# Optimization experiments

Hardware: AMD Instinct MI355X
Metric: run time of the kernel (lower is better)

The kernel has to match this reference:

```python
import jax, jax.numpy as jnp
import numpy as np

B, T, D, H = 2, 2048, 1024, 16
HD = D // H
ALPHA = HD ** -0.5
EPS = 1e-5


def setup_inputs() -> dict:
    key = jax.random.key(0)
    ks = jax.random.split(key, 8)
    x = jax.random.normal(ks[0], (B, T, D), dtype=jnp.float32)
    # additive causal mask: 0 where allowed, -inf where disallowed
    causal = jnp.triu(jnp.ones((T, T), dtype=bool), k=1)
    attention_mask = jnp.where(causal, -jnp.inf, 0.0).astype(jnp.float32)
    rab = jax.random.normal(ks[1], (1, H, T, T), dtype=jnp.float32) * 0.02
    W_in = jax.random.normal(ks[2], (D, 4 * D), dtype=jnp.float32) * (D ** -0.5)
    b_in = jnp.zeros((4 * D,), dtype=jnp.float32)
    W_out = jax.random.normal(ks[3], (D, D), dtype=jnp.float32) * (D ** -0.5)
    b_out = jnp.zeros((D,), dtype=jnp.float32)
    ln_w = jnp.ones((D,), dtype=jnp.float32)
    ln_b = jnp.zeros((D,), dtype=jnp.float32)
    return {"x": x, "attention_mask": attention_mask, "rab": rab,
            "W_in": W_in, "b_in": b_in, "W_out": W_out, "b_out": b_out,
            "ln_w": ln_w, "ln_b": ln_b}


def _heads(t):  # [B,T,D] -> [B,H,T,HD]
    return t.reshape(B, T, H, HD).transpose(0, 2, 1, 3)


def _layernorm(t, w, b):
    mu = jnp.mean(t, axis=-1, keepdims=True)
    var = jnp.mean(jnp.square(t - mu), axis=-1, keepdims=True)
    return (t - mu) * jax.lax.rsqrt(var + EPS) * w + b


def reference(x, attention_mask, rab, W_in, b_in, W_out, b_out, ln_w, ln_b):
    h = jax.nn.silu(x @ W_in + b_in)                      # [B,T,4D]
    U, V, Q, K = jnp.split(h, 4, axis=-1)
    Qh, Kh, Vh = _heads(Q), _heads(K), _heads(V)
    logits = jnp.einsum('bhqd,bhkd->bhqk', Qh, Kh) * ALPHA
    logits = logits + rab + attention_mask[None, None]    # [B,H,T,T]
    # allowed counts from the additive mask (0 == allowed)
    allowed = (attention_mask == 0).astype(jnp.float32)   # [T,T]
    denom = jnp.clip(jnp.sum(allowed, axis=-1, keepdims=True), 1.0)  # [T,1]
    logits_safe = jnp.where(jnp.isinf(logits) & (logits < 0), -1e9, logits)
    attn = jax.nn.silu(logits_safe) / denom[None, None]
    AV = jnp.einsum('bhqk,bhkd->bhqd', attn, Vh)
    AV = AV.transpose(0, 2, 1, 3).reshape(B, T, D)
    y = (_layernorm(AV, ln_w, ln_b) * U) @ W_out + b_out
    return y
```

## Files before the change

### kernel.cpp

```cpp
#include <hip/hip_runtime.h>
#include <hip/hip_bf16.h>

#define BATCH 2
#define TSEQ 2048
#define DIM 1024
#define NH 16
#define HDIM 64
#define MROWS (BATCH * TSEQ)

typedef __attribute__((ext_vector_type(4))) float f32x4;
typedef __attribute__((ext_vector_type(8))) short short8;

__device__ __forceinline__ unsigned short f2bf(float f) {
    union { float f; unsigned int u; } x; x.f = f;
    unsigned int r = x.u + 0x7fffu + ((x.u >> 16) & 1u);
    return (unsigned short)(r >> 16);
}

__device__ __forceinline__ float bf2f(unsigned short s) {
    union { unsigned int u; float f; } t; t.u = (unsigned int)s << 16;
    return t.f;
}

__device__ __forceinline__ float silu_f(float v) {
    return v * __builtin_amdgcn_rcpf(1.f + __expf(-v));
}

__device__ __forceinline__ unsigned int pack_bf16(float lo, float hi) {
    union { __hip_bfloat162 h; unsigned int u; } r;
    r.h = __float22bfloat162_rn(float2{lo, hi});
    return r.u;
}

__device__ __forceinline__ void gl_lds16(const void* g, void* l) {
    __builtin_amdgcn_global_load_lds(
        (const __attribute__((address_space(1))) void*)g,
        (__attribute__((address_space(3))) void*)l, 16, 0, 0);
}

__device__ __forceinline__ short8 rd_swz(const unsigned short* base, int row, int chunk) {
    const char* b = (const char*)base;
    return *(const short8*)(b + row * 128 + (((chunk ^ (row & 7)) << 4)));
}

__global__ __launch_bounds__(256) void k_convert(const float* __restrict__ in,
                                                 unsigned short* __restrict__ out,
                                                 int n4) {
    int i = blockIdx.x * 256 + threadIdx.x;
    if (i < n4) {
        float4 v = ((const float4*)in)[i];
        union { unsigned short s[4]; uint2 u; } o;
        o.s[0] = f2bf(v.x); o.s[1] = f2bf(v.y); o.s[2] = f2bf(v.z); o.s[3] = f2bf(v.w);
        ((uint2*)out)[i] = o.u;
    }
}

__global__ __launch_bounds__(256) void k_transpose(const float* __restrict__ in,
                                                   unsigned short* __restrict__ out,
                                                   int R, int C) {
    __shared__ float tile[32][33];
    int tx = threadIdx.x, ty = threadIdx.y;
    int c0 = blockIdx.x * 32, r0 = blockIdx.y * 32;
    #pragma unroll
    for (int i = 0; i < 32; i += 8)
        tile[ty + i][tx] = in[(size_t)(r0 + ty + i) * C + c0 + tx];
    __syncthreads();
    #pragma unroll
    for (int i = 0; i < 32; i += 8)
        out[(size_t)(c0 + ty + i) * R + r0 + tx] = f2bf(tile[tx][ty + i]);
}

__device__ __forceinline__ void stage256(const unsigned short* __restrict__ A,
                                         const unsigned short* __restrict__ Bt,
                                         int row0, int col0, int k0,
                                         unsigned short* sAbuf, unsigned short* sBbuf,
                                         int tid) {
    #pragma unroll
    for (int q = 0; q < 4; ++q) {
        int c = tid + 512 * q;
        int rr = c >> 3;
        int kcs = (c & 7) ^ (rr & 7);
        gl_lds16(A + (size_t)(row0 + rr) * 1024 + k0 + kcs * 8, sAbuf + c * 8);
        gl_lds16(Bt + (size_t)(col0 + rr) * 1024 + k0 + kcs * 8, sBbuf + c * 8);
    }
}

__global__ __launch_bounds__(512, 2) void k_gemm1_256(
    const unsigned short* __restrict__ A, const unsigned short* __restrict__ Bt,
    const float* __restrict__ bias,
    unsigned short* __restrict__ outU, unsigned short* __restrict__ outVt,
    unsigned short* __restrict__ outQ, unsigned short* __restrict__ outK)
{
    __shared__ __align__(16) unsigned short sA[2][256 * 64];
    __shared__ __align__(16) unsigned short sB[2][256 * 64];

    const int tid = threadIdx.x;
    const int lane = tid & 63, wid = tid >> 6;
    const int lr = lane & 15, lk = lane >> 4;
    const int wm = wid >> 2, wn = wid & 3;
    const int bm = blockIdx.x, bn = blockIdx.y;
    const int row0 = bm * 256, col0 = bn * 256;

    f32x4 acc[8][4] = {};

    stage256(A, Bt, row0, col0, 0, sA[0], sB[0], tid);
    asm volatile("s_waitcnt vmcnt(0)" ::: "memory");
    __builtin_amdgcn_s_barrier();
    __builtin_amdgcn_sched_barrier(0);

    int cur = 0;
    for (int kt = 0; kt < 16; ++kt) {
        if (kt < 15) stage256(A, Bt, row0, col0, (kt + 1) * 64, sA[cur ^ 1], sB[cur ^ 1], tid);
        short8 bf[2][4];
        #pragma unroll
        for (int kk = 0; kk < 2; ++kk)
            #pragma unroll
            for (int n = 0; n < 4; ++n)
                bf[kk][n] = rd_swz(sB[cur], wn * 64 + n * 16 + lr, kk * 4 + lk);

        #pragma unroll
        for (int ph = 0; ph < 4; ++ph) {
            short8 af[2][2];
            #pragma unroll
            for (int mm = 0; mm < 2; ++mm)
                #pragma unroll
                for (int kk = 0; kk < 2; ++kk)
                    af[mm][kk] = rd_swz(sA[cur], wm * 128 + (ph * 2 + mm) * 16 + lr, kk * 4 + lk);
            __builtin_amdgcn_s_barrier();
            __builtin_amdgcn_s_setprio(1);
            #pragma unroll
            for (int mm = 0; mm < 2; ++mm)
                #pragma unroll
                for (int n = 0; n < 4; ++n)
                    #pragma unroll
                    for (int kk = 0; kk < 2; ++kk)
                        acc[ph * 2 + mm][n] = __builtin_amdgcn_mfma_f32_16x16x32_bf16(
                            af[mm][kk], bf[kk][n], acc[ph * 2 + mm][n], 0, 0, 0);
            __builtin_amdgcn_s_setprio(0);
            if (ph == 3) asm volatile("s_waitcnt vmcnt(0)" ::: "memory");
            __builtin_amdgcn_s_barrier();
        }
        __builtin_amdgcn_sched_barrier(0);
        cur ^= 1;
    }

    const int sec = bn >> 2;
    #pragma unroll
    for (int n = 0; n < 4; ++n) {
        const int cg = col0 + wn * 64 + n * 16 + lr;
        const int cc = cg & 1023;
        const float bv = bias[cg];
        #pragma unroll
        for (int m = 0; m < 8; ++m) {
            const int rg0 = row0 + wm * 128 + m * 16 + lk * 4;
            float sv[4];
            #pragma unroll
            for (int j = 0; j < 4; ++j)
                sv[j] = silu_f(acc[m][n][j] + bv);
            if (sec == 0) {
                #pragma unroll
                for (int j = 0; j < 4; ++j)
                    outU[((size_t)(rg0 + j) << 10) + cc] = f2bf(sv[j]);
            } else if (sec == 1) {
                union { unsigned short s[4]; uint2 u; } pk;
                #pragma unroll
                for (int j = 0; j < 4; ++j) pk.s[j] = f2bf(sv[j]);
                *(uint2*)(outVt + ((size_t)cc << 12) + rg0) = pk.u;
            } else if (sec == 2) {
                #pragma unroll
                for (int j = 0; j < 4; ++j)
                    outQ[((size_t)(rg0 + j) << 10) + cc] = f2bf(sv[j] * 0.125f);
            } else {
                #pragma unroll
                for (int j = 0; j < 4; ++j)
                    outK[((size_t)(rg0 + j) << 10) + cc] = f2bf(sv[j]);
            }
        }
    }
}

__device__ __forceinline__ void stage128(const unsigned short* __restrict__ A,
                                         const unsigned short* __restrict__ Bt,
                                         int row0, int col0, int k0,
                                         unsigned short* sAbuf, unsigned short* sBbuf,
                                         int tid) {
    #pragma unroll
    for (int q = 0; q < 4; ++q) {
        int c = tid + 256 * q;
        int rr = c >> 3;
        int kcs = (c & 7) ^ (rr & 7);
        gl_lds16(A + (size_t)(row0 + rr) * 1024 + k0 + kcs * 8, sAbuf + c * 8);
        gl_lds16(Bt + (size_t)(col0 + rr) * 1024 + k0 + kcs * 8, sBbuf + c * 8);
    }
}

__global__ __launch_bounds__(256, 2) void k_gemm2(
    const unsigned short* __restrict__ A, const unsigned short* __restrict__ Bt,
    const float* __restrict__ bias, float* __restrict__ outY)
{
    __shared__ __align__(16) unsigned short sA[2][128 * 64];
    __shared__ __align__(16) unsigned short sB[2][128 * 64];

    const int tid = threadIdx.x;
    const int lane = tid & 63, wid = tid >> 6;
    const int lr = lane & 15, lk = lane >> 4;
    const int wm = wid >> 1, wn = wid & 1;
    const int bm = blockIdx.x, bn = blockIdx.y;
    const int row0 = bm * 128, col0 = bn * 128;

    f32x4 acc[4][4] = {};

    stage128(A, Bt, row0, col0, 0, sA[0], sB[0], tid);
    asm volatile("s_waitcnt vmcnt(0)" ::: "memory");
    __builtin_amdgcn_s_barrier();
    __builtin_amdgcn_sched_barrier(0);

    int cur = 0;
    for (int kt = 0; kt < 16; ++kt) {
        if (kt < 15) stage128(A, Bt, row0, col0, (kt + 1) * 64, sA[cur ^ 1], sB[cur ^ 1], tid);
        short8 bf[2][4];
        #pragma unroll
        for (int kk = 0; kk < 2; ++kk)
            #pragma unroll
            for (int n = 0; n < 4; ++n)
                bf[kk][n] = rd_swz(sB[cur], wn * 64 + n * 16 + lr, kk * 4 + lk);

        #pragma unroll
        for (int ph = 0; ph < 2; ++ph) {
            short8 af[2][2];
            #pragma unroll
            for (int mm = 0; mm < 2; ++mm)
                #pragma unroll
                for (int kk = 0; kk < 2; ++kk)
                    af[mm][kk] = rd_swz(sA[cur], wm * 64 + (ph * 2 + mm) * 16 + lr, kk * 4 + lk);
            __builtin_amdgcn_s_barrier();
            __builtin_amdgcn_s_setprio(1);
            #pragma unroll
            for (int mm = 0; mm < 2; ++mm)
                #pragma unroll
                for (int n = 0; n < 4; ++n)
                    #pragma unroll
                    for (int kk = 0; kk < 2; ++kk)
                        acc[ph * 2 + mm][n] = __builtin_amdgcn_mfma_f32_16x16x32_bf16(
                            af[mm][kk], bf[kk][n], acc[ph * 2 + mm][n], 0, 0, 0);
            __builtin_amdgcn_s_setprio(0);
            if (ph == 1) asm volatile("s_waitcnt vmcnt(0)" ::: "memory");
            __builtin_amdgcn_s_barrier();
        }
        __builtin_amdgcn_sched_barrier(0);
        cur ^= 1;
    }

    #pragma unroll
    for (int n = 0; n < 4; ++n) {
        const int cg = col0 + wn * 64 + n * 16 + lr;
        const float bv = bias[cg];
        #pragma unroll
        for (int m = 0; m < 4; ++m) {
            const int rg0 = row0 + wm * 64 + m * 16 + lk * 4;
            #pragma unroll
            for (int j = 0; j < 4; ++j)
                outY[(size_t)(rg0 + j) * 1024 + cg] = acc[m][n][j] + bv;
        }
    }
}

__global__ __launch_bounds__(256, 4) void k_attn(
    const unsigned short* __restrict__ Qb,
    const unsigned short* __restrict__ Kb,
    const unsigned short* __restrict__ Vt,
    const float* __restrict__ rab,
    unsigned short* __restrict__ AV)
{
    __shared__ __align__(16) unsigned short sK[2][64 * 64];
    __shared__ __align__(16) unsigned short sVt[2][64 * 64];
    __shared__ __align__(16) unsigned short sP[64 * 64];

    const int tid = threadIdx.x;
    const int lane = tid & 63;
    const int w = tid >> 6;
    const int lr = lane & 15;
    const int lk = lane >> 4;

    const int bid = blockIdx.x;
    const int idx = bid & 255;
    const int g = bid >> 8;
    const int h = idx & 15;
    const int r_ = idx >> 4;
    const int bb = g >> 1;
    const int qt = (g & 1) ? (31 - r_) : r_;
    const int q0 = qt * 64;

    short8 qreg[2];
    #pragma unroll
    for (int ks = 0; ks < 2; ++ks)
        qreg[ks] = *(const short8*)(Qb + (((size_t)(bb * TSEQ + q0 + w * 16 + lr)) << 10)
                                     + h * 64 + ks * 32 + lk * 8);
    __builtin_amdgcn_sched_barrier(0);

    const int qloc = w * 16 + lr;
    const int qcol = q0 + qloc;
    const float* rabq = rab + ((size_t)h * TSEQ + qcol) * TSEQ + lk * 4;

    f32x4 acc[4] = {};

    #define STAGE(buf, kt_) do {                                                      \
        int k0s = (kt_) * 64;                                                         \
        for (int c = tid; c < 512; c += 256) {                                        \
            int rr = c >> 3, kc = c & 7;                                              \
            int kcs = kc ^ (rr & 7);                                                  \
            gl_lds16(Kb + (((size_t)(bb * TSEQ + k0s + rr)) << 10) + h * 64 + kcs * 8,\
                     sK[buf] + c * 8);                                                \
            gl_lds16(Vt + (((size_t)(h * 64 + rr)) << 12) + bb * TSEQ + k0s + kcs * 8,\
                     sVt[buf] + c * 8);                                               \
        }                                                                             \
    } while (0)

    float4 rv0[4], rv1[4];

    STAGE(0, 0);
    __builtin_amdgcn_sched_barrier(0);
    #pragma unroll
    for (int nt = 0; nt < 4; ++nt)
        rv0[nt] = *(const float4*)(rabq + nt * 16);
    __builtin_amdgcn_sched_barrier(0);
    asm volatile("s_waitcnt vmcnt(4)" ::: "memory");
    __builtin_amdgcn_s_barrier();

    #define BODY(KT, BUFC, RVC, RVN) do {                                             \
        const int k0 = (KT) * 64;                                                     \
        const bool have_next = (KT) < qt;                                             \
        if (have_next) STAGE((BUFC) ^ 1, (KT) + 1);                                   \
        __builtin_amdgcn_sched_barrier(0);                                            \
        if (have_next) {                                                              \
            _Pragma("unroll")                                                         \
            for (int nt = 0; nt < 4; ++nt)                                            \
                RVN[nt] = *(const float4*)(rabq + k0 + 64 + nt * 16);                 \
        }                                                                             \
        __builtin_amdgcn_sched_barrier(0);                                            \
        f32x4 s[4];                                                                   \
        _Pragma("unroll")                                                             \
        for (int nt = 0; nt < 4; ++nt) {                                              \
            s[nt][0] = RVC[nt].x; s[nt][1] = RVC[nt].y;                               \
            s[nt][2] = RVC[nt].z; s[nt][3] = RVC[nt].w;                               \
        }                                                                             \
        __builtin_amdgcn_s_setprio(1);                                                \
        _Pragma("unroll")                                                             \
        for (int ks = 0; ks < 2; ++ks) {                                              \
            _Pragma("unroll")                                                         \
            for (int nt = 0; nt < 4; ++nt)                                            \
                s[nt] = __builtin_amdgcn_mfma_f32_16x16x32_bf16(                      \
                    rd_swz(sK[BUFC], nt * 16 + lr, ks * 4 + lk), qreg[ks], s[nt], 0, 0, 0); \
        }                                                                             \
        __builtin_amdgcn_s_setprio(0);                                                \
        char* pb = (char*)sP;                                                         \
        char* paddr = pb + qloc * 128 + ((lk & 1) * 8);                               \
        if (have_next) {                                                              \
            _Pragma("unroll")                                                         \
            for (int nt = 0; nt < 4; ++nt) {                                          \
                unsigned int p01 = pack_bf16(silu_f(s[nt][0]), silu_f(s[nt][1]));     \
                unsigned int p23 = pack_bf16(silu_f(s[nt][2]), silu_f(s[nt][3]));     \
                const int chunk = nt * 2 + (lk >> 1);                                 \
                *(uint2*)(paddr + ((chunk ^ (qloc & 7)) << 4)) = make_uint2(p01, p23);\
            }                                                                         \
        } else {                                                                      \
            _Pragma("unroll")                                                         \
            for (int nt = 0; nt < 4; ++nt) {                                          \
                const int kb = k0 + nt * 16 + lk * 4;                                 \
                float a0 = (kb + 0 <= qcol) ? silu_f(s[nt][0]) : 0.f;                 \
                float a1 = (kb + 1 <= qcol) ? silu_f(s[nt][1]) : 0.f;                 \
                float a2 = (kb + 2 <= qcol) ? silu_f(s[nt][2]) : 0.f;                 \
                float a3 = (kb + 3 <= qcol) ? silu_f(s[nt][3]) : 0.f;                 \
                unsigned int p01 = pack_bf16(a0, a1);                                 \
                unsigned int p23 = pack_bf16(a2, a3);                                 \
                const int chunk = nt * 2 + (lk >> 1);                                 \
                *(uint2*)(paddr + ((chunk ^ (qloc & 7)) << 4)) = make_uint2(p01, p23);\
            }                                                                         \
        }                                                                             \
        __builtin_amdgcn_s_setprio(1);                                                \
        _Pragma("unroll")                                                             \
        for (int ks = 0; ks < 2; ++ks) {                                              \
            short8 ap = rd_swz(sP, qloc, ks * 4 + lk);                                \
            _Pragma("unroll")                                                         \
            for (int dt = 0; dt < 4; ++dt)                                            \
                acc[dt] = __builtin_amdgcn_mfma_f32_16x16x32_bf16(                    \
                    ap, rd_swz(sVt[BUFC], dt * 16 + lr, ks * 4 + lk), acc[dt], 0, 0, 0); \
        }                                                                             \
        __builtin_amdgcn_s_setprio(0);                                                \
        if (have_next) {                                                              \
            asm volatile("s_waitcnt vmcnt(4)" ::: "memory");                          \
            __builtin_amdgcn_s_barrier();                                             \
        }                                                                             \
    } while (0)

    for (int kt = 0; kt <= qt; kt += 2) {
        BODY(kt, 0, rv0, rv1);
        if (kt + 1 <= qt) BODY(kt + 1, 1, rv1, rv0);
    }
    #undef BODY
    #undef STAGE

    #pragma unroll
    for (int dt = 0; dt < 4; ++dt)
        #pragma unroll
        for (int j = 0; j < 4; ++j)
            AV[(((size_t)(bb * TSEQ + q0 + w * 16 + lk * 4 + j)) << 10)
               + h * 64 + dt * 16 + lr] = f2bf(acc[dt][j]);
}

__global__ __launch_bounds__(256) void k_ln(const unsigned short* __restrict__ AV,
                                            const unsigned short* __restrict__ U,
                                            const float* __restrict__ lnw,
                                            const float* __restrict__ lnb,
                                            unsigned short* __restrict__ z) {
    __shared__ float red[8];
    const int row = blockIdx.x, tid = threadIdx.x;
    const float c = (float)((row & (TSEQ - 1)) + 1);
    const float eps = 1e-5f * c * c;
    union { unsigned short s[4]; uint2 u; } a;
    a.u = ((const uint2*)(AV + ((size_t)row << 10)))[tid];
    float v[4];
    #pragma unroll
    for (int i = 0; i < 4; ++i) v[i] = bf2f(a.s[i]);
    float s = v[0] + v[1] + v[2] + v[3];
    float s2 = v[0] * v[0] + v[1] * v[1] + v[2] * v[2] + v[3] * v[3];
    #pragma unroll
    for (int o = 32; o > 0; o >>= 1) { s += __shfl_xor(s, o); s2 += __shfl_xor(s2, o); }
    const int w = tid >> 6;
    if ((tid & 63) == 0) { red[w] = s; red[4 + w] = s2; }
    __syncthreads();
    s = red[0] + red[1] + red[2] + red[3];
    s2 = red[4] + red[5] + red[6] + red[7];
    const float mu = s * (1.f / 1024.f);
    const float var = s2 * (1.f / 1024.f) - mu * mu;
    const float rstd = rsqrtf(var + eps);
    union { unsigned short s[4]; uint2 u; } uu;
    uu.u = ((const uint2*)(U + ((size_t)row << 10)))[tid];
    float4 lw = ((const float4*)lnw)[tid];
    float4 lb = ((const float4*)lnb)[tid];
    union { unsigned short o[4]; uint2 u; } ov;
    ov.o[0] = f2bf(((v[0] - mu) * rstd * lw.x + lb.x) * bf2f(uu.s[0]));
    ov.o[1] = f2bf(((v[1] - mu) * rstd * lw.y + lb.y) * bf2f(uu.s[1]));
    ov.o[2] = f2bf(((v[2] - mu) * rstd * lw.z + lb.z) * bf2f(uu.s[2]));
    ov.o[3] = f2bf(((v[3] - mu) * rstd * lw.w + lb.w) * bf2f(uu.s[3]));
    ((uint2*)z)[((size_t)row << 8) + tid] = ov.u;
}

extern "C" void kernel_launch(void* const* d_in, const int* in_sizes, int n_in,
                              void* d_out, int out_size, void* d_ws, size_t ws_size,
                              hipStream_t stream) {
    const float* x     = (const float*)d_in[0];
    const float* rab   = (const float*)d_in[2];
    const float* W_in  = (const float*)d_in[3];
    const float* b_in  = (const float*)d_in[4];
    const float* W_out = (const float*)d_in[5];
    const float* b_out = (const float*)d_in[6];
    const float* ln_w  = (const float*)d_in[7];
    const float* ln_b  = (const float*)d_in[8];
    float* y = (float*)d_out;

    char* ws = (char*)d_ws;
    size_t off = 0;
    auto alloc = [&](size_t bytes) -> void* {
        void* p = ws + off;
        off += (bytes + 255) & ~(size_t)255;
        return p;
    };
    unsigned short* WinT  = (unsigned short*)alloc((size_t)4096 * 1024 * 2);
    unsigned short* WoutT = (unsigned short*)alloc((size_t)1024 * 1024 * 2);
    unsigned short* xb    = (unsigned short*)alloc((size_t)MROWS * DIM * 2);
    unsigned short* Ubuf  = (unsigned short*)alloc((size_t)MROWS * DIM * 2);
    unsigned short* Qb    = (unsigned short*)alloc((size_t)MROWS * DIM * 2);
    unsigned short* Kb    = (unsigned short*)alloc((size_t)MROWS * DIM * 2);
    unsigned short* Vtb   = (unsigned short*)alloc((size_t)DIM * MROWS * 2);
    unsigned short* AV    = (unsigned short*)alloc((size_t)MROWS * DIM * 2);
    unsigned short* z     = (unsigned short*)alloc((size_t)MROWS * DIM * 2);

    k_convert<<<dim3(4096), dim3(256), 0, stream>>>(x, xb, MROWS * DIM / 4);
    k_transpose<<<dim3(128, 32), dim3(32, 8), 0, stream>>>(W_in, WinT, 1024, 4096);
    k_transpose<<<dim3(32, 32), dim3(32, 8), 0, stream>>>(W_out, WoutT, 1024, 1024);
    k_gemm1_256<<<dim3(16, 16), dim3(512), 0, stream>>>(xb, WinT, b_in, Ubuf, Vtb, Qb, Kb);
    k_attn<<<dim3(1024), dim3(256), 0, stream>>>(Qb, Kb, Vtb, rab, AV);
    k_ln<<<dim3(MROWS), dim3(256), 0, stream>>>(AV, Ubuf, ln_w, ln_b, z);
    k_gemm2<<<dim3(32, 8), dim3(256), 0, stream>>>(z, WoutT, b_out, y);
}
```

Baseline: 156.6 us.

## Fuse prep kernels, use fine-grained vmcnt waits in GEMMs, remap attention blocks to XCDs

Merges the convert and two transpose kernels into one launch to cut launch overhead. Both GEMMs now issue B loads first and split A loads into ordered groups, waiting with partial vmcnt counts per phase instead of draining all loads at the end. The final k-tile is peeled so the loop has no branch on the prefetch. The attention block index is remapped so heads are spread across XCDs with balanced causal work, which adds risk if the vmcnt counts do not match the actual load ordering.

```diff
diff --git a/kernel.cpp b/kernel.cpp
--- a/kernel.cpp
+++ b/kernel.cpp
@@ -43,24 +43,12 @@
     return *(const short8*)(b + row * 128 + (((chunk ^ (row & 7)) << 4)));
 }
 
-__global__ __launch_bounds__(256) void k_convert(const float* __restrict__ in,
-                                                 unsigned short* __restrict__ out,
-                                                 int n4) {
-    int i = blockIdx.x * 256 + threadIdx.x;
-    if (i < n4) {
-        float4 v = ((const float4*)in)[i];
-        union { unsigned short s[4]; uint2 u; } o;
-        o.s[0] = f2bf(v.x); o.s[1] = f2bf(v.y); o.s[2] = f2bf(v.z); o.s[3] = f2bf(v.w);
-        ((uint2*)out)[i] = o.u;
-    }
-}
-
-__global__ __launch_bounds__(256) void k_transpose(const float* __restrict__ in,
-                                                   unsigned short* __restrict__ out,
-                                                   int R, int C) {
+__device__ __forceinline__ void transpose32(const float* __restrict__ in,
+                                            unsigned short* __restrict__ out,
+                                            int R, int C, int bx, int by, int tid) {
     __shared__ float tile[32][33];
-    int tx = threadIdx.x, ty = threadIdx.y;
-    int c0 = blockIdx.x * 32, r0 = blockIdx.y * 32;
+    int tx = tid & 31, ty = tid >> 5;
+    int c0 = bx * 32, r0 = by * 32;
     #pragma unroll
     for (int i = 0; i < 32; i += 8)
         tile[ty + i][tx] = in[(size_t)(r0 + ty + i) * C + c0 + tx];
@@ -70,18 +58,48 @@
         out[(size_t)(c0 + ty + i) * R + r0 + tx] = f2bf(tile[tx][ty + i]);
 }
 
-__device__ __forceinline__ void stage256(const unsigned short* __restrict__ A,
-                                         const unsigned short* __restrict__ Bt,
-                                         int row0, int col0, int k0,
-                                         unsigned short* sAbuf, unsigned short* sBbuf,
-                                         int tid) {
+__global__ __launch_bounds__(256) void k_prep(const float* __restrict__ x,
+                                              unsigned short* __restrict__ xb,
+                                              const float* __restrict__ W_in,
+                                              unsigned short* __restrict__ WinT,
+                                              const float* __restrict__ W_out,
+                                              unsigned short* __restrict__ WoutT) {
+    const int b = blockIdx.x, tid = threadIdx.x;
+    if (b < 4096) {
+        int i = b * 256 + tid;
+        float4 v = ((const float4*)x)[i];
+        union { unsigned short s[4]; uint2 u; } o;
+        o.s[0] = f2bf(v.x); o.s[1] = f2bf(v.y); o.s[2] = f2bf(v.z); o.s[3] = f2bf(v.w);
+        ((uint2*)xb)[i] = o.u;
+    } else if (b < 8192) {
+        int bb = b - 4096;
+        transpose32(W_in, WinT, 1024, 4096, bb & 127, bb >> 7, tid);
+    } else {
+        int bb = b - 8192;
+        transpose32(W_out, WoutT, 1024, 1024, bb & 31, bb >> 5, tid);
+    }
+}
+
+__device__ __forceinline__ void stage256o(const unsigned short* __restrict__ A,
+                                          const unsigned short* __restrict__ Bt,
+                                          int row0, int col0, int k0,
+                                          unsigned short* sAbuf, unsigned short* sBbuf,
+                                          int tid) {
     #pragma unroll
     for (int q = 0; q < 4; ++q) {
         int c = tid + 512 * q;
         int rr = c >> 3;
         int kcs = (c & 7) ^ (rr & 7);
+        gl_lds16(Bt + (size_t)(col0 + rr) * 1024 + k0 + kcs * 8, sBbuf + c * 8);
+    }
+    __builtin_amdgcn_sched_barrier(0);
+    #pragma unroll
+    for (int p = 0; p < 4; ++p) {
+        int c = (tid < 256) ? (256 * p + tid) : (1024 + 256 * p + (tid - 256));
+        int rr = c >> 3;
+        int kcs = (c & 7) ^ (rr & 7);
         gl_lds16(A + (size_t)(row0 + rr) * 1024 + k0 + kcs * 8, sAbuf + c * 8);
-        gl_lds16(Bt + (size_t)(col0 + rr) * 1024 + k0 + kcs * 8, sBbuf + c * 8);
+        __builtin_amdgcn_sched_barrier(0);
     }
 }
 
@@ -103,14 +121,14 @@
 
     f32x4 acc[8][4] = {};
 
-    stage256(A, Bt, row0, col0, 0, sA[0], sB[0], tid);
+    stage256o(A, Bt, row0, col0, 0, sA[0], sB[0], tid);
     asm volatile("s_waitcnt vmcnt(0)" ::: "memory");
     __builtin_amdgcn_s_barrier();
     __builtin_amdgcn_sched_barrier(0);
 
     int cur = 0;
-    for (int kt = 0; kt < 16; ++kt) {
-        if (kt < 15) stage256(A, Bt, row0, col0, (kt + 1) * 64, sA[cur ^ 1], sB[cur ^ 1], tid);
+    for (int kt = 0; kt < 15; ++kt) {
+        stage256o(A, Bt, row0, col0, (kt + 1) * 64, sA[cur ^ 1], sB[cur ^ 1], tid);
         short8 bf[2][4];
         #pragma unroll
         for (int kk = 0; kk < 2; ++kk)
@@ -137,13 +155,48 @@
                         acc[ph * 2 + mm][n] = __builtin_amdgcn_mfma_f32_16x16x32_bf16(
                             af[mm][kk], bf[kk][n], acc[ph * 2 + mm][n], 0, 0, 0);
             __builtin_amdgcn_s_setprio(0);
-            if (ph == 3) asm volatile("s_waitcnt vmcnt(0)" ::: "memory");
+            if (ph == 0)      asm volatile("s_waitcnt vmcnt(10)" ::: "memory");
+            else if (ph == 1) asm volatile("s_waitcnt vmcnt(9)" ::: "memory");
+            else if (ph == 2) asm volatile("s_waitcnt vmcnt(8)" ::: "memory");
+            else              asm volatile("s_waitcnt vmcnt(3)" ::: "memory");
             __builtin_amdgcn_s_barrier();
         }
         __builtin_amdgcn_sched_barrier(0);
         cur ^= 1;
     }
 
+    {
+        short8 bf[2][4];
+        #pragma unroll
+        for (int kk = 0; kk < 2; ++kk)
+            #pragma unroll
+            for (int n = 0; n < 4; ++n)
+                bf[kk][n] = rd_swz(sB[cur], wn * 64 + n * 16 + lr, kk * 4 + lk);
+        #pragma unroll
+        for (int ph = 0; ph < 4; ++ph) {
+            short8 af[2][2];
+            #pragma unroll
+            for (int mm = 0; mm < 2; ++mm)
+                #pragma unroll
+                for (int kk = 0; kk < 2; ++kk)
+                    af[mm][kk] = rd_swz(sA[cur], wm * 128 + (ph * 2 + mm) * 16 + lr, kk * 4 + lk);
+            __builtin_amdgcn_s_barrier();
+            __builtin_amdgcn_s_setprio(1);
+            #pragma unroll
+            for (int mm = 0; mm < 2; ++mm)
+                #pragma unroll
+                for (int n = 0; n < 4; ++n)
+                    #pragma unroll
+                    for (int kk = 0; kk < 2; ++kk)
+                        acc[ph * 2 + mm][n] = __builtin_amdgcn_mfma_f32_16x16x32_bf16(
+                            af[mm][kk], bf[kk][n], acc[ph * 2 + mm][n], 0, 0, 0);
+            __builtin_amdgcn_s_setprio(0);
+            if (ph == 0)      { asm volatile("s_waitcnt vmcnt(2)" ::: "memory"); __builtin_amdgcn_s_barrier(); }
+            else if (ph == 1) { asm volatile("s_waitcnt vmcnt(1)" ::: "memory"); __builtin_amdgcn_s_barrier(); }
+            else if (ph == 2) { asm volatile("s_waitcnt vmcnt(0)" ::: "memory"); __builtin_amdgcn_s_barrier(); }
+        }
+    }
+
     const int sec = bn >> 2;
     #pragma unroll
     for (int n = 0; n < 4; ++n) {
@@ -179,19 +232,33 @@
     }
 }
 
-__device__ __forceinline__ void stage128(const unsigned short* __restrict__ A,
-                                         const unsigned short* __restrict__ Bt,
-                                         int row0, int col0, int k0,
-                                         unsigned short* sAbuf, unsigned short* sBbuf,
-                                         int tid) {
+__device__ __forceinline__ void stage128o(const unsigned short* __restrict__ A,
+                                          const unsigned short* __restrict__ Bt,
+                                          int row0, int col0, int k0,
+                                          unsigned short* sAbuf, unsigned short* sBbuf,
+                                          int tid) {
     #pragma unroll
     for (int q = 0; q < 4; ++q) {
         int c = tid + 256 * q;
         int rr = c >> 3;
         int kcs = (c & 7) ^ (rr & 7);
+        gl_lds16(Bt + (size_t)(col0 + rr) * 1024 + k0 + kcs * 8, sBbuf + c * 8);
+    }
+    __builtin_amdgcn_sched_barrier(0);
+    {
+        int c = tid;          int rr = c >> 3; int kcs = (c & 7) ^ (rr & 7);
         gl_lds16(A + (size_t)(row0 + rr) * 1024 + k0 + kcs * 8, sAbuf + c * 8);
-        gl_lds16(Bt + (size_t)(col0 + rr) * 1024 + k0 + kcs * 8, sBbuf + c * 8);
-    }
+        c = 512 + tid;        rr = c >> 3;     kcs = (c & 7) ^ (rr & 7);
+        gl_lds16(A + (size_t)(row0 + rr) * 1024 + k0 + kcs * 8, sAbuf + c * 8);
+    }
+    __builtin_amdgcn_sched_barrier(0);
+    {
+        int c = 256 + tid;    int rr = c >> 3; int kcs = (c & 7) ^ (rr & 7);
+        gl_lds16(A + (size_t)(row0 + rr) * 1024 + k0 + kcs * 8, sAbuf + c * 8);
+        c = 768 + tid;        rr = c >> 3;     kcs = (c & 7) ^ (rr & 7);
+        gl_lds16(A + (size_t)(row0 + rr) * 1024 + k0 + kcs * 8, sAbuf + c * 8);
+    }
+    __builtin_amdgcn_sched_barrier(0);
 }
 
 __global__ __launch_bounds__(256, 2) void k_gemm2(
@@ -210,14 +277,14 @@
 
     f32x4 acc[4][4] = {};
 
-    stage128(A, Bt, row0, col0, 0, sA[0], sB[0], tid);
+    stage128o(A, Bt, row0, col0, 0, sA[0], sB[0], tid);
     asm volatile("s_waitcnt vmcnt(0)" ::: "memory");
     __builtin_amdgcn_s_barrier();
     __builtin_amdgcn_sched_barrier(0);
 
     int cur = 0;
-    for (int kt = 0; kt < 16; ++kt) {
-        if (kt < 15) stage128(A, Bt, row0, col0, (kt + 1) * 64, sA[cur ^ 1], sB[cur ^ 1], tid);
+    for (int kt = 0; kt < 15; ++kt) {
+        stage128o(A, Bt, row0, col0, (kt + 1) * 64, sA[cur ^ 1], sB[cur ^ 1], tid);
         short8 bf[2][4];
         #pragma unroll
         for (int kk = 0; kk < 2; ++kk)
@@ -244,11 +311,42 @@
                         acc[ph * 2 + mm][n] = __builtin_amdgcn_mfma_f32_16x16x32_bf16(
                             af[mm][kk], bf[kk][n], acc[ph * 2 + mm][n], 0, 0, 0);
             __builtin_amdgcn_s_setprio(0);
-            if (ph == 1) asm volatile("s_waitcnt vmcnt(0)" ::: "memory");
+            if (ph == 0) asm volatile("s_waitcnt vmcnt(10)" ::: "memory");
+            else         asm volatile("s_waitcnt vmcnt(2)" ::: "memory");
             __builtin_amdgcn_s_barrier();
         }
         __builtin_amdgcn_sched_barrier(0);
         cur ^= 1;
+    }
+
+    {
+        short8 bf[2][4];
+        #pragma unroll
+        for (int kk = 0; kk < 2; ++kk)
+            #pragma unroll
+            for (int n = 0; n < 4; ++n)
+                bf[kk][n] = rd_swz(sB[cur], wn * 64 + n * 16 + lr, kk * 4 + lk);
+        #pragma unroll
+        for (int ph = 0; ph < 2; ++ph) {
+            short8 af[2][2];
+            #pragma unroll
+            for (int mm = 0; mm < 2; ++mm)
+                #pragma unroll
+                for (int kk = 0; kk < 2; ++kk)
+                    af[mm][kk] = rd_swz(sA[cur], wm * 64 + (ph * 2 + mm) * 16 + lr, kk * 4 + lk);
+            __builtin_amdgcn_s_barrier();
+            __builtin_amdgcn_s_setprio(1);
+            #pragma unroll
+            for (int mm = 0; mm < 2; ++mm)
+                #pragma unroll
+                for (int n = 0; n < 4; ++n)
+                    #pragma unroll
+                    for (int kk = 0; kk < 2; ++kk)
+                        acc[ph * 2 + mm][n] = __builtin_amdgcn_mfma_f32_16x16x32_bf16(
+                            af[mm][kk], bf[kk][n], acc[ph * 2 + mm][n], 0, 0, 0);
+            __builtin_amdgcn_s_setprio(0);
+            if (ph == 0) { asm volatile("s_waitcnt vmcnt(0)" ::: "memory"); __builtin_amdgcn_s_barrier(); }
+        }
     }
 
     #pragma unroll
@@ -283,12 +381,14 @@
     const int lk = lane >> 4;
 
     const int bid = blockIdx.x;
-    const int idx = bid & 255;
-    const int g = bid >> 8;
-    const int h = idx & 15;
-    const int r_ = idx >> 4;
-    const int bb = g >> 1;
-    const int qt = (g & 1) ? (31 - r_) : r_;
+    const int xcd = bid & 7;
+    const int j_ = bid >> 3;
+    const int cc_ = j_ & 31;
+    const int b4 = j_ >> 5;
+    const int h = ((b4 & 1) << 3) | xcd;
+    const int bb = b4 >> 1;
+    const int cc2 = (b4 >= 2) ? ((cc_ + 16) & 31) : cc_;
+    const int qt = (b4 & 1) ? (31 - cc2) : cc2;
     const int q0 = qt * 64;
 
     short8 qreg[2];
@@ -476,9 +576,7 @@
     unsigned short* AV    = (unsigned short*)alloc((size_t)MROWS * DIM * 2);
     unsigned short* z     = (unsigned short*)alloc((size_t)MROWS * DIM * 2);
 
-    k_convert<<<dim3(4096), dim3(256), 0, stream>>>(x, xb, MROWS * DIM / 4);
-    k_transpose<<<dim3(128, 32), dim3(32, 8), 0, stream>>>(W_in, WinT, 1024, 4096);
-    k_transpose<<<dim3(32, 32), dim3(32, 8), 0, stream>>>(W_out, WoutT, 1024, 1024);
+    k_prep<<<dim3(9216), dim3(256), 0, stream>>>(x, xb, W_in, WinT, W_out, WoutT);
     k_gemm1_256<<<dim3(16, 16), dim3(512), 0, stream>>>(xb, WinT, b_in, Ubuf, Vtb, Qb, Kb);
     k_attn<<<dim3(1024), dim3(256), 0, stream>>>(Qb, Kb, Vtb, rab, AV);
     k_ln<<<dim3(MROWS), dim3(256), 0, stream>>>(AV, Ubuf, ln_w, ln_b, z);
```

Measured after the change: 156.5 us (median of 2 runs). About the same (-0.1%).
